# Optimization experiments

Measured on AMD Instinct MI355X. Metric: run time of the kernel, lower is better.

## Reference

```python
import jax, jax.numpy as jnp
import numpy as np

B, T, IN, H, L, OUT, PRED, FN = 512, 96, 64, 512, 2, 1, 24, 32


def setup_inputs() -> dict:
    key = jax.random.key(0)
    ks = jax.random.split(key, 12)
    sc = 0.02
    n = lambda i, shape: jax.random.normal(ks[i], shape, jnp.float32) * sc
    return {
        "x": jax.random.normal(ks[0], (B, T, IN), jnp.float32),
        "station_id": jax.random.randint(ks[1], (B,), 0, 26, jnp.int32),
        "W_hidden": n(2, (H, IN)), "b_hidden": jnp.zeros((H,), jnp.float32),
        "embed": n(3, (26, H)),
        "W_ih": n(4, (L, 4 * H, H)), "W_hh": n(5, (L, 4 * H, H)),
        "b_ih": jnp.zeros((L, 4 * H), jnp.float32), "b_hh": jnp.zeros((L, 4 * H), jnp.float32),
        "conv_W": n(6, (FN, T - 1)), "conv_b": jnp.zeros((FN,), jnp.float32),
        "W1": n(7, (FN, H)), "b1": jnp.zeros((FN,), jnp.float32),
        "W2": n(8, (H, H + FN)), "b2": jnp.zeros((H,), jnp.float32),
        "W_out": n(9, (T * OUT, H)), "b_out": jnp.zeros((T * OUT,), jnp.float32),
    }


def _lstm(xc, W_ih, W_hh, b_ih, b_hh):
    # xc: [B, T, H]; multi-layer LSTM, PyTorch gate order i,f,g,o
    n_layers = W_ih.shape[0]
    h0 = jnp.zeros((n_layers, xc.shape[0], W_hh.shape[-1]), xc.dtype)

    def step(carry, xt):
        h, c = carry  # [L, B, H]
        inp = xt
        hs, cs = [], []
        for l in range(n_layers):
            g = inp @ W_ih[l].T + h[l] @ W_hh[l].T + b_ih[l] + b_hh[l]
            i, f, gg, o = jnp.split(g, 4, axis=-1)
            cn = jax.nn.sigmoid(f) * c[l] + jax.nn.sigmoid(i) * jnp.tanh(gg)
            hn = jax.nn.sigmoid(o) * jnp.tanh(cn)
            hs.append(hn); cs.append(cn)
            inp = hn
        return (jnp.stack(hs), jnp.stack(cs)), inp  # emit last-layer h

    _, outs = jax.lax.scan(step, (h0, h0), jnp.swapaxes(xc, 0, 1))
    return jnp.swapaxes(outs, 0, 1)  # [B, T, H] last-layer hidden states


def reference(x, station_id, W_hidden, b_hidden, embed, W_ih, W_hh, b_ih, b_hh,
              conv_W, conv_b, W1, b1, W2, b2, W_out, b_out):
    b, t, _ = x.shape
    hdim = W_hidden.shape[0]
    fn = conv_W.shape[0]
    xc = jax.nn.relu(x @ W_hidden.T + b_hidden)
    xc = xc + embed[station_id][:, None, :]
    hs_seq = _lstm(xc, W_ih, W_hh, b_ih, b_hh)          # [B, T, H]
    Hmat = jax.nn.relu(hs_seq[:, :-1, :])                # [B, T-1, H]
    htt = hs_seq[:, -1, :]                               # [B, H]
    # Conv2d(1, FN, (T-1, 1)) over [B,1,T-1,H] == contraction over time
    conv = jax.nn.relu(jnp.einsum('bth,ft->bfh', Hmat, conv_W) + conv_b[None, :, None])
    # original does .view(-1, feat_size, filter_num): raw reshape, not transpose
    feat = conv.reshape(b, hdim, fn)                     # [B, H, FN]
    w = (htt @ W1.T + b1)[:, None, :]                    # [B, 1, FN]
    alpha = jax.nn.sigmoid(jnp.sum(feat * w, axis=2))    # [B, H]
    v = jnp.sum(alpha[:, :, None] * feat, axis=1)        # [B, FN]
    new_ht = jnp.concatenate([htt, v], axis=1) @ W2.T + b2
    ypred = (new_ht @ W_out.T + b_out)[:, -PRED * OUT:]
    return ypred
```

## Files before the change

kernel.cpp:

```cpp
#include <hip/hip_runtime.h>
#include <math.h>

namespace {

constexpr int B = 512, T = 96, IN = 64, H = 512, G4 = 2048;
constexpr int FN = 32, KC = 544, NPRED = 24, TM1 = T - 1;
constexpr int BH = B * H;

typedef __attribute__((ext_vector_type(8))) short s8v;
typedef __attribute__((ext_vector_type(16))) float f16v;

__device__ __forceinline__ float sigf(float x) { return 1.0f / (1.0f + __expf(-x)); }
__device__ __forceinline__ float tanhfast(float x) {
  x = fminf(fmaxf(x, -15.f), 15.f);
  float e = __expf(2.0f * x);
  return (e - 1.0f) / (e + 1.0f);
}
__device__ __forceinline__ unsigned short bf16_rne(float f) {
  unsigned u = __float_as_uint(f);
  u += 0x7fffu + ((u >> 16) & 1u);
  return (unsigned short)(u >> 16);
}
__device__ __forceinline__ void split8(const float4& x, const float4& y, s8v& hi, s8v& lo) {
  float vs[8] = {x.x, x.y, x.z, x.w, y.x, y.y, y.z, y.w};
#pragma unroll
  for (int j = 0; j < 8; ++j) {
    unsigned ub = __float_as_uint(vs[j]);
    hi[j] = (short)(ub >> 16);
    lo[j] = (short)bf16_rne(vs[j] - __uint_as_float(ub & 0xffff0000u));
  }
}

__global__ __launch_bounds__(256) void k_xc(
    const float* __restrict__ x, const int* __restrict__ sid,
    const float* __restrict__ Wh, const float* __restrict__ bh,
    const float* __restrict__ emb, float* __restrict__ planes) {
  constexpr int RWS = 64;
  int gid = blockIdx.x;
  int half = gid & 1;
  int row0 = (gid >> 1) * RWS;
  int tid = threadIdx.x;
  int h = half * 256 + tid;
  __shared__ float sx[RWS][IN];
  {
    const float4* xsrc = (const float4*)(x + (size_t)row0 * IN);
    float4* sdst = (float4*)(&sx[0][0]);
    for (int i = tid; i < RWS * IN / 4; i += 256) sdst[i] = xsrc[i];
  }
  float4 w[16];
  const float* wr = Wh + (size_t)h * IN;
#pragma unroll
  for (int j = 0; j < 16; ++j) w[j] = *(const float4*)(wr + j * 4);
  float b0 = bh[h];
  const float* ep = emb + h;
  __syncthreads();
#pragma unroll 2
  for (int r = 0; r < RWS; ++r) {
    float a0 = b0, a1 = 0.f, a2 = 0.f, a3 = 0.f;
#pragma unroll
    for (int j = 0; j < 16; ++j) {
      float4 xv = *(const float4*)(&sx[r][j * 4]);
      a0 = fmaf(xv.x, w[j].x, a0);
      a1 = fmaf(xv.y, w[j].y, a1);
      a2 = fmaf(xv.z, w[j].z, a2);
      a3 = fmaf(xv.w, w[j].w, a3);
    }
    float acc = (a0 + a1) + (a2 + a3);
    int row = row0 + r;
    int bb = row / T, t = row % T;
    float v = fmaxf(acc, 0.f) + ep[(size_t)sid[bb] * H];
    planes[((size_t)t * B + bb) * H + h] = v;
  }
}

__global__ __launch_bounds__(256) void k_wswz(
    const float* __restrict__ Wih, const float* __restrict__ Whh,
    short* __restrict__ WFhi, short* __restrict__ WFlo) {
  int g = blockIdx.x * 256 + threadIdx.x;
  int lane = g & 63;
  int fi = g >> 6;
  int nt = fi & 3, kt = (fi >> 2) & 63, ng = (fi >> 8) & 15, layer = fi >> 12;
  int row = nt * H + ng * 32 + (lane & 31);
  int kk = kt * 16 + (lane >> 5) * 8;
  const float* src = (kk < H) ? (Wih + ((size_t)layer * G4 + row) * H + kk)
                              : (Whh + ((size_t)layer * G4 + row) * H + (kk - H));
  float4 f0 = *(const float4*)src, f1 = *(const float4*)(src + 4);
  s8v hi, lo;
  split8(f0, f1, hi, lo);
  size_t o = (size_t)fi * 512 + lane * 8;
  *(s8v*)(WFhi + o) = hi;
  *(s8v*)(WFlo + o) = lo;
}

__global__ __launch_bounds__(256, 1) void k_step(
    int tt, float* __restrict__ planes, const short* __restrict__ WFhi,
    const short* __restrict__ WFlo, short* __restrict__ hFhi,
    short* __restrict__ hFlo, const float* __restrict__ bih,
    const float* __restrict__ bhh, float* __restrict__ c0,
    float* __restrict__ c1) {
  int gid = blockIdx.x;
  int xcd = gid & 7;
  int u = gid >> 3;
  int combo = xcd * 4 + (u & 3);
  int layer = combo >> 4;
  if (layer ? (tt == 0) : (tt == T)) return;
  int ng = combo & 15;
  int b0 = (u >> 2) * 64;
  int step = layer ? (tt - 1) : tt;
  int tid = threadIdx.x, lane = tid & 63, wk = tid >> 6;
  int l31 = lane & 31, lh = lane >> 5;

  __shared__ float comb[4][4][32][32];

  const float* bi = bih + (size_t)layer * G4;
  const float* bh2 = bhh + (size_t)layer * G4;
  float* cbuf = layer ? c1 : c0;

  int rpar = (step - 1) & 1;
  const float* xbase = nullptr;
  const short *abhi = nullptr, *ablo = nullptr;
  if (layer == 0 && wk < 2) {
    xbase = planes + (size_t)step * BH + (size_t)(b0 + l31) * H + wk * 256 + lh * 8;
  } else {
    int src = (layer == 0) ? 0 : ((wk < 2) ? 0 : 1);
    int par = (layer == 0) ? rpar : ((wk < 2) ? (step & 1) : rpar);
    int kk0 = wk * 16 - ((layer == 0 || wk >= 2) ? 32 : 0);
    size_t o = ((((size_t)src * 2 + par) * 32 + kk0) * H + (b0 + l31)) * 16 + lh * 8;
    abhi = hFhi + o;
    ablo = hFlo + o;
  }

  float bias[4];
#pragma unroll
  for (int nt = 0; nt < 4; ++nt) {
    int r = nt * H + ng * 32 + l31;
    bias[nt] = bi[r] + bh2[r];
  }

  const size_t wstep = 4 * 512;
  const size_t wbase0 = ((size_t)(layer * 16 + ng) * 64 + wk * 16) * wstep + (size_t)lane * 8;
  const size_t astep = (size_t)H * 16;

  f16v acc[2][4];
#pragma unroll
  for (int rt = 0; rt < 2; ++rt)
#pragma unroll
    for (int nt = 0; nt < 4; ++nt)
#pragma unroll
      for (int e = 0; e < 16; ++e) acc[rt][nt][e] = 0.f;

  s8v a0h0, a0l0, a0h1, a0l1, b0h0, b0h1, b0h2, b0h3, b0l0, b0l1, b0l2, b0l3;
  s8v a1h0, a1l0, a1h1, a1l1, b1h0, b1h1, b1h2, b1h3, b1l0, b1l1, b1l2, b1l3;
  s8v a2h0, a2l0, a2h1, a2l1, b2h0, b2h1, b2h2, b2h3, b2l0, b2l1, b2l2, b2l3;

#define LOADW_(kq, bh0, bh1, bh2, bh3, bl0, bl1, bl2, bl3)          \
  {                                                                 \
    size_t wo = wbase0 + (size_t)(kq) * wstep;                      \
    bh0 = *(const s8v*)(WFhi + wo);                                 \
    bh1 = *(const s8v*)(WFhi + wo + 512);                           \
    bh2 = *(const s8v*)(WFhi + wo + 1024);                          \
    bh3 = *(const s8v*)(WFhi + wo + 1536);                          \
    bl0 = *(const s8v*)(WFlo + wo);                                 \
    bl1 = *(const s8v*)(WFlo + wo + 512);                           \
    bl2 = *(const s8v*)(WFlo + wo + 1024);                          \
    bl3 = *(const s8v*)(WFlo + wo + 1536);                          \
  }
#define LOADA_(kq, ah0, al0, ah1, al1)                              \
  {                                                                 \
    if (xbase) {                                                    \
      const float* ap = xbase + (kq) * 16;                          \
      float4 f0 = *(const float4*)ap, f1 = *(const float4*)(ap + 4);\
      split8(f0, f1, ah0, al0);                                     \
      const float* aq = ap + 32 * H;                                \
      float4 g0 = *(const float4*)aq, g1 = *(const float4*)(aq + 4);\
      split8(g0, g1, ah1, al1);                                     \
    } else {                                                        \
      const short* ph = abhi + (size_t)(kq) * astep;                \
      const short* pl = ablo + (size_t)(kq) * astep;                \
      ah0 = *(const s8v*)(ph);                                      \
      al0 = *(const s8v*)(pl);                                      \
      ah1 = *(const s8v*)(ph + 512);                                \
      al1 = *(const s8v*)(pl + 512);                                \
    }                                                               \
  }
#define MFMA3R_(rt, ah, al, bh0, bh1, bh2, bh3, bl0, bl1, bl2, bl3)                        \
  {                                                                                        \
    acc[rt][0] = __builtin_amdgcn_mfma_f32_32x32x16_bf16(ah, bh0, acc[rt][0], 0, 0, 0);    \
    acc[rt][1] = __builtin_amdgcn_mfma_f32_32x32x16_bf16(ah, bh1, acc[rt][1], 0, 0, 0);    \
    acc[rt][2] = __builtin_amdgcn_mfma_f32_32x32x16_bf16(ah, bh2, acc[rt][2], 0, 0, 0);    \
    acc[rt][3] = __builtin_amdgcn_mfma_f32_32x32x16_bf16(ah, bh3, acc[rt][3], 0, 0, 0);    \
    acc[rt][0] = __builtin_amdgcn_mfma_f32_32x32x16_bf16(ah, bl0, acc[rt][0], 0, 0, 0);    \
    acc[rt][1] = __builtin_amdgcn_mfma_f32_32x32x16_bf16(ah, bl1, acc[rt][1], 0, 0, 0);    \
    acc[rt][2] = __builtin_amdgcn_mfma_f32_32x32x16_bf16(ah, bl2, acc[rt][2], 0, 0, 0);    \
    acc[rt][3] = __builtin_amdgcn_mfma_f32_32x32x16_bf16(ah, bl3, acc[rt][3], 0, 0, 0);    \
    acc[rt][0] = __builtin_amdgcn_mfma_f32_32x32x16_bf16(al, bh0, acc[rt][0], 0, 0, 0);    \
    acc[rt][1] = __builtin_amdgcn_mfma_f32_32x32x16_bf16(al, bh1, acc[rt][1], 0, 0, 0);    \
    acc[rt][2] = __builtin_amdgcn_mfma_f32_32x32x16_bf16(al, bh2, acc[rt][2], 0, 0, 0);    \
    acc[rt][3] = __builtin_amdgcn_mfma_f32_32x32x16_bf16(al, bh3, acc[rt][3], 0, 0, 0);    \
  }
#define MFMA6_(ah0, al0, ah1, al1, bh0, bh1, bh2, bh3, bl0, bl1, bl2, bl3)  \
  {                                                                         \
    MFMA3R_(0, ah0, al0, bh0, bh1, bh2, bh3, bl0, bl1, bl2, bl3);           \
    MFMA3R_(1, ah1, al1, bh0, bh1, bh2, bh3, bl0, bl1, bl2, bl3);           \
  }

  LOADA_(0, a0h0, a0l0, a0h1, a0l1);
  LOADW_(0, b0h0, b0h1, b0h2, b0h3, b0l0, b0l1, b0l2, b0l3);
  LOADA_(1, a1h0, a1l0, a1h1, a1l1);
  LOADW_(1, b1h0, b1h1, b1h2, b1h3, b1l0, b1l1, b1l2, b1l3);
  LOADA_(2, a2h0, a2l0, a2h1, a2l1);
  LOADW_(2, b2h0, b2h1, b2h2, b2h3, b2l0, b2l1, b2l2, b2l3);
#pragma unroll 1
  for (int kp = 0; kp < 5; ++kp) {
    int kq = kp * 3;
    MFMA6_(a0h0, a0l0, a0h1, a0l1, b0h0, b0h1, b0h2, b0h3, b0l0, b0l1, b0l2, b0l3);
    LOADA_(kq + 3, a0h0, a0l0, a0h1, a0l1);
    LOADW_(kq + 3, b0h0, b0h1, b0h2, b0h3, b0l0, b0l1, b0l2, b0l3);
    MFMA6_(a1h0, a1l0, a1h1, a1l1, b1h0, b1h1, b1h2, b1h3, b1l0, b1l1, b1l2, b1l3);
    if (kp < 4) {
      LOADA_(kq + 4, a1h0, a1l0, a1h1, a1l1);
      LOADW_(kq + 4, b1h0, b1h1, b1h2, b1h3, b1l0, b1l1, b1l2, b1l3);
    }
    MFMA6_(a2h0, a2l0, a2h1, a2l1, b2h0, b2h1, b2h2, b2h3, b2l0, b2l1, b2l2, b2l3);
    if (kp < 4) {
      LOADA_(kq + 5, a2h0, a2l0, a2h1, a2l1);
      LOADW_(kq + 5, b2h0, b2h1, b2h2, b2h3, b2l0, b2l1, b2l2, b2l3);
    }
  }
  MFMA6_(a0h0, a0l0, a0h1, a0l1, b0h0, b0h1, b0h2, b0h3, b0l0, b0l1, b0l2, b0l3);
#undef LOADW_
#undef LOADA_
#undef MFMA3R_
#undef MFMA6_

#pragma unroll
  for (int rt = 0; rt < 2; ++rt) {
    if (rt) __syncthreads();
#pragma unroll
    for (int nt = 0; nt < 4; ++nt)
#pragma unroll
      for (int r = 0; r < 16; ++r) {
        int row = (r & 3) + 8 * (r >> 2) + 4 * lh;
        comb[nt][wk][row][l31] = acc[rt][nt][r];
      }
    __syncthreads();
    int b0p = b0 + rt * 32;
#pragma unroll
    for (int rr = 0; rr < 4; ++rr) {
      int r = wk * 4 + rr;
      int row = (r & 3) + 8 * (r >> 2) + 4 * lh;
      float g[4];
#pragma unroll
      for (int nt = 0; nt < 4; ++nt) {
        float p0 = comb[nt][0][row][l31];
        float p1 = comb[nt][1][row][l31];
        float p2 = comb[nt][2][row][l31];
        float p3 = comb[nt][3][row][l31];
        g[nt] = (p0 + p1) + (p2 + p3) + bias[nt];
      }
      size_t coff = (size_t)(b0p + row) * H + ng * 32 + l31;
      float cp = cbuf[coff];
      float cn = sigf(g[1]) * cp + sigf(g[0]) * tanhfast(g[2]);
      float hn = sigf(g[3]) * tanhfast(cn);
      cbuf[coff] = cn;
      int brow = b0p + row;
      int hcol = ng * 32 + l31;
      size_t o = ((((size_t)layer * 2 + (step & 1)) * 32 + (hcol >> 4)) * H + brow) * 16 + (hcol & 15);
      unsigned ub = __float_as_uint(hn);
      hFhi[o] = (short)(ub >> 16);
      hFlo[o] = (short)bf16_rne(hn - __uint_as_float(ub & 0xffff0000u));
      if (layer) planes[(size_t)step * BH + (size_t)brow * H + hcol] = hn;
    }
  }
}

__global__ __launch_bounds__(256) void k_conv(
    const float* __restrict__ hs, const float* __restrict__ cW,
    const float* __restrict__ cb, float* __restrict__ feat) {
  int b = blockIdx.x >> 2;
  int h0 = (blockIdx.x & 3) * 128;
  int tid = threadIdx.x;
  __shared__ float sW[TM1][FN];
  for (int i = tid; i < TM1 * FN; i += 256) sW[i >> 5][i & 31] = cW[(i & 31) * TM1 + (i >> 5)];
  __syncthreads();
  int hl = tid & 127, fg = (tid >> 7) * 16;
  float acc[16];
#pragma unroll
  for (int j = 0; j < 16; ++j) acc[j] = cb[fg + j];
  const float* hp = hs + (size_t)b * H + h0 + hl;
  for (int t = 0; t < TM1; ++t) {
    float v = fmaxf(hp[(size_t)t * BH], 0.f);
#pragma unroll
    for (int j = 0; j < 16; ++j) acc[j] = fmaf(v, sW[t][fg + j], acc[j]);
  }
#pragma unroll
  for (int j = 0; j < 16; ++j)
    feat[(size_t)b * (FN * H) + (size_t)(fg + j) * H + h0 + hl] = fmaxf(acc[j], 0.f);
}

__global__ __launch_bounds__(256) void k_attn(
    const float* __restrict__ hs, const float* __restrict__ feat,
    const float* __restrict__ W1, const float* __restrict__ b1,
    const float* __restrict__ W2, const float* __restrict__ b2,
    const float* __restrict__ Wout, const float* __restrict__ bout,
    float* __restrict__ out) {
  int b = blockIdx.x, tid = threadIdx.x;
  __shared__ float sh[H], sa[H], snew[H], sw[FN], sv[FN], red[256];
  const float* htt = hs + (size_t)(T - 1) * BH + (size_t)b * H;
  for (int i = tid; i < H; i += 256) sh[i] = htt[i];
  __syncthreads();
  {
    int f = tid >> 3, sl = tid & 7;
    const float* w1 = W1 + (size_t)f * H;
    float p = 0.f;
    for (int k = sl * 64; k < sl * 64 + 64; ++k) p = fmaf(sh[k], w1[k], p);
    p += __shfl_xor(p, 1); p += __shfl_xor(p, 2); p += __shfl_xor(p, 4);
    if (sl == 0) sw[f] = p + b1[f];
  }
  __syncthreads();
  const float* fb = feat + (size_t)b * (FN * H);
  for (int i = tid; i < H; i += 256) {
    const float* fr = fb + (size_t)i * FN;
    float p = 0.f;
#pragma unroll
    for (int j = 0; j < FN; j += 4) {
      float4 fv = *(const float4*)(fr + j);
      p = fmaf(fv.x, sw[j], p);
      p = fmaf(fv.y, sw[j + 1], p);
      p = fmaf(fv.z, sw[j + 2], p);
      p = fmaf(fv.w, sw[j + 3], p);
    }
    sa[i] = sigf(p);
  }
  __syncthreads();
  {
    int j = tid & 31, isl = tid >> 5;
    float p = 0.f;
    for (int i = isl * 64; i < isl * 64 + 64; ++i) p = fmaf(sa[i], fb[(size_t)i * FN + j], p);
    red[tid] = p;
  }
  __syncthreads();
  if (tid < 128) red[tid] += red[tid + 128];
  __syncthreads();
  if (tid < 64) red[tid] += red[tid + 64];
  __syncthreads();
  if (tid < 32) sv[tid] = red[tid] + red[tid + 32];
  __syncthreads();
  for (int h = tid; h < H; h += 256) {
    const float* w2 = W2 + (size_t)h * KC;
    float p = b2[h];
#pragma unroll 4
    for (int k = 0; k < H; k += 4) {
      float4 wv = *(const float4*)(w2 + k);
      float4 shv = *(const float4*)(sh + k);
      p = fmaf(shv.x, wv.x, p);
      p = fmaf(shv.y, wv.y, p);
      p = fmaf(shv.z, wv.z, p);
      p = fmaf(shv.w, wv.w, p);
    }
#pragma unroll
    for (int j = 0; j < FN; j += 4) {
      float4 wv = *(const float4*)(w2 + H + j);
      p = fmaf(sv[j], wv.x, p);
      p = fmaf(sv[j + 1], wv.y, p);
      p = fmaf(sv[j + 2], wv.z, p);
      p = fmaf(sv[j + 3], wv.w, p);
    }
    snew[h] = p;
  }
  __syncthreads();
  if (tid < NPRED * 8) {
    int p = tid >> 3, sl = tid & 7;
    const float* wo = Wout + (size_t)(T - NPRED + p) * H;
    float sacc = 0.f;
    for (int k = sl * 64; k < sl * 64 + 64; ++k) sacc = fmaf(snew[k], wo[k], sacc);
    sacc += __shfl_xor(sacc, 1); sacc += __shfl_xor(sacc, 2); sacc += __shfl_xor(sacc, 4);
    if (sl == 0) out[(size_t)b * NPRED + p] = sacc + bout[T - NPRED + p];
  }
}

}

extern "C" void kernel_launch(void* const* d_in, const int* in_sizes, int n_in,
                              void* d_out, int out_size, void* d_ws, size_t ws_size,
                              hipStream_t stream) {
  const float* x    = (const float*)d_in[0];
  const int*   sid  = (const int*)d_in[1];
  const float* Wh   = (const float*)d_in[2];
  const float* bh   = (const float*)d_in[3];
  const float* emb  = (const float*)d_in[4];
  const float* Wih  = (const float*)d_in[5];
  const float* Whh  = (const float*)d_in[6];
  const float* bih  = (const float*)d_in[7];
  const float* bhh  = (const float*)d_in[8];
  const float* cW   = (const float*)d_in[9];
  const float* cb   = (const float*)d_in[10];
  const float* W1   = (const float*)d_in[11];
  const float* b1   = (const float*)d_in[12];
  const float* W2   = (const float*)d_in[13];
  const float* b2   = (const float*)d_in[14];
  const float* Wout = (const float*)d_in[15];
  const float* bout = (const float*)d_in[16];
  float* out = (float*)d_out;

  constexpr size_t HFE = (size_t)2 * 2 * 32 * H * 16;
  float* planes = (float*)d_ws;
  short* WFhi = (short*)(planes + (size_t)T * BH);
  short* WFlo = WFhi + (size_t)8192 * 512;
  short* hFhi = WFlo + (size_t)8192 * 512;
  short* hFlo = hFhi + HFE;
  float* cst = (float*)(hFlo + HFE);
  float* c0 = cst;
  float* c1 = cst + BH;
  float* feat = c1 + BH;
  size_t need = (size_t)T * BH * 4 + (size_t)8192 * 512 * 2 * 2 + HFE * 2 * 2 +
                2 * (size_t)BH * 4 + (size_t)B * FN * H * 4;
  if (ws_size < need) return;

  hipMemsetAsync(hFhi, 0, HFE * 2 * 2 + 2 * (size_t)BH * 4, stream);
  k_xc<<<(B * T / 64) * 2, 256, 0, stream>>>(x, sid, Wh, bh, emb, planes);
  k_wswz<<<2048, 256, 0, stream>>>(Wih, Whh, WFhi, WFlo);

  for (int tt = 0; tt <= T; ++tt)
    k_step<<<256, 256, 0, stream>>>(tt, planes, WFhi, WFlo, hFhi, hFlo, bih, bhh, c0, c1);

  k_conv<<<B * 4, 256, 0, stream>>>(planes, cW, cb, feat);
  k_attn<<<B, 256, 0, stream>>>(planes, feat, W1, b1, W2, b2, Wout, bout, out);
}
```

Before: 2.324 ms.

## Transpose W2 for coalesced reads, fuse attention passes, widen xc per-thread work

Adds a kernel that transposes W2 into a k-group-major float4 layout, so the W2 matvec in the attention kernel reads coalesced across threads instead of strided by row. The alpha computation and the weighted feature sum are fused into a single pass that uses shuffle reductions plus a float4 tree reduction, which removes the sa buffer and a second read of feat. k_xc now computes both halves of H per thread, so each x row is loaded into shared memory once instead of twice, at the cost of higher register use. These kernels are small next to the 97 sequential LSTM step launches.

```diff
diff --git a/kernel.cpp b/kernel.cpp
--- a/kernel.cpp
+++ b/kernel.cpp
@@ -36,40 +36,48 @@
     const float* __restrict__ Wh, const float* __restrict__ bh,
     const float* __restrict__ emb, float* __restrict__ planes) {
   constexpr int RWS = 64;
-  int gid = blockIdx.x;
-  int half = gid & 1;
-  int row0 = (gid >> 1) * RWS;
+  int row0 = blockIdx.x * RWS;
   int tid = threadIdx.x;
-  int h = half * 256 + tid;
-  __shared__ float sx[RWS][IN];
+  __shared__ __align__(16) float sx[RWS][IN];
   {
     const float4* xsrc = (const float4*)(x + (size_t)row0 * IN);
     float4* sdst = (float4*)(&sx[0][0]);
     for (int i = tid; i < RWS * IN / 4; i += 256) sdst[i] = xsrc[i];
   }
-  float4 w[16];
-  const float* wr = Wh + (size_t)h * IN;
-#pragma unroll
-  for (int j = 0; j < 16; ++j) w[j] = *(const float4*)(wr + j * 4);
-  float b0 = bh[h];
-  const float* ep = emb + h;
+  float4 w0[16], w1[16];
+  const float* wr0 = Wh + (size_t)tid * IN;
+  const float* wr1 = Wh + (size_t)(tid + 256) * IN;
+#pragma unroll
+  for (int j = 0; j < 16; ++j) {
+    w0[j] = *(const float4*)(wr0 + j * 4);
+    w1[j] = *(const float4*)(wr1 + j * 4);
+  }
+  float bb0 = bh[tid], bb1 = bh[tid + 256];
   __syncthreads();
 #pragma unroll 2
   for (int r = 0; r < RWS; ++r) {
-    float a0 = b0, a1 = 0.f, a2 = 0.f, a3 = 0.f;
+    float a00 = bb0, a01 = 0.f, a02 = 0.f, a03 = 0.f;
+    float a10 = bb1, a11 = 0.f, a12 = 0.f, a13 = 0.f;
 #pragma unroll
     for (int j = 0; j < 16; ++j) {
       float4 xv = *(const float4*)(&sx[r][j * 4]);
-      a0 = fmaf(xv.x, w[j].x, a0);
-      a1 = fmaf(xv.y, w[j].y, a1);
-      a2 = fmaf(xv.z, w[j].z, a2);
-      a3 = fmaf(xv.w, w[j].w, a3);
-    }
-    float acc = (a0 + a1) + (a2 + a3);
+      a00 = fmaf(xv.x, w0[j].x, a00);
+      a01 = fmaf(xv.y, w0[j].y, a01);
+      a02 = fmaf(xv.z, w0[j].z, a02);
+      a03 = fmaf(xv.w, w0[j].w, a03);
+      a10 = fmaf(xv.x, w1[j].x, a10);
+      a11 = fmaf(xv.y, w1[j].y, a11);
+      a12 = fmaf(xv.z, w1[j].z, a12);
+      a13 = fmaf(xv.w, w1[j].w, a13);
+    }
+    float acc0 = (a00 + a01) + (a02 + a03);
+    float acc1 = (a10 + a11) + (a12 + a13);
     int row = row0 + r;
     int bb = row / T, t = row % T;
-    float v = fmaxf(acc, 0.f) + ep[(size_t)sid[bb] * H];
-    planes[((size_t)t * B + bb) * H + h] = v;
+    const float* eb = emb + (size_t)sid[bb] * H;
+    size_t o = ((size_t)t * B + bb) * H;
+    planes[o + tid] = fmaxf(acc0, 0.f) + eb[tid];
+    planes[o + tid + 256] = fmaxf(acc1, 0.f) + eb[tid + 256];
   }
 }
 
@@ -92,6 +100,13 @@
   *(s8v*)(WFlo + o) = lo;
 }
 
+__global__ __launch_bounds__(256) void k_w2t(
+    const float* __restrict__ W2, float* __restrict__ W2T4) {
+  int g = blockIdx.x * 256 + threadIdx.x;
+  int h = g / KC, k = g % KC;
+  W2T4[((size_t)(k >> 2) * H + h) * 4 + (k & 3)] = W2[g];
+}
+
 __global__ __launch_bounds__(256, 1) void k_step(
     int tt, float* __restrict__ planes, const short* __restrict__ WFhi,
     const short* __restrict__ WFlo, short* __restrict__ hFhi,
@@ -175,12 +190,12 @@
       float4 g0 = *(const float4*)aq, g1 = *(const float4*)(aq + 4);\
       split8(g0, g1, ah1, al1);                                     \
     } else {                                                        \
-      const short* ph = abhi + (size_t)(kq) * astep;                \
-      const short* pl = ablo + (size_t)(kq) * astep;                \
-      ah0 = *(const s8v*)(ph);                                      \
-      al0 = *(const s8v*)(pl);                                      \
-      ah1 = *(const s8v*)(ph + 512);                                \
-      al1 = *(const s8v*)(pl + 512);                                \
+      const short* ph_ = abhi + (size_t)(kq) * astep;               \
+      const short* pl_ = ablo + (size_t)(kq) * astep;               \
+      ah0 = *(const s8v*)(ph_);                                     \
+      al0 = *(const s8v*)(pl_);                                     \
+      ah1 = *(const s8v*)(ph_ + 512);                               \
+      al1 = *(const s8v*)(pl_ + 512);                               \
     }                                                               \
   }
 #define MFMA3R_(rt, ah, al, bh0, bh1, bh2, bh3, bl0, bl1, bl2, bl3)                        \
@@ -301,11 +316,12 @@
 __global__ __launch_bounds__(256) void k_attn(
     const float* __restrict__ hs, const float* __restrict__ feat,
     const float* __restrict__ W1, const float* __restrict__ b1,
-    const float* __restrict__ W2, const float* __restrict__ b2,
+    const float* __restrict__ W2T4, const float* __restrict__ b2,
     const float* __restrict__ Wout, const float* __restrict__ bout,
     float* __restrict__ out) {
   int b = blockIdx.x, tid = threadIdx.x;
-  __shared__ float sh[H], sa[H], snew[H], sw[FN], sv[FN], red[256];
+  __shared__ __align__(16) float sh[H], snew[H], sw[FN], sv[FN];
+  __shared__ __align__(16) float4 red4[32][8];
   const float* htt = hs + (size_t)(T - 1) * BH + (size_t)b * H;
   for (int i = tid; i < H; i += 256) sh[i] = htt[i];
   __syncthreads();
@@ -319,52 +335,60 @@
   }
   __syncthreads();
   const float* fb = feat + (size_t)b * (FN * H);
-  for (int i = tid; i < H; i += 256) {
-    const float* fr = fb + (size_t)i * FN;
-    float p = 0.f;
-#pragma unroll
-    for (int j = 0; j < FN; j += 4) {
-      float4 fv = *(const float4*)(fr + j);
-      p = fmaf(fv.x, sw[j], p);
-      p = fmaf(fv.y, sw[j + 1], p);
-      p = fmaf(fv.z, sw[j + 2], p);
-      p = fmaf(fv.w, sw[j + 3], p);
-    }
-    sa[i] = sigf(p);
-  }
-  __syncthreads();
-  {
-    int j = tid & 31, isl = tid >> 5;
-    float p = 0.f;
-    for (int i = isl * 64; i < isl * 64 + 64; ++i) p = fmaf(sa[i], fb[(size_t)i * FN + j], p);
-    red[tid] = p;
-  }
-  __syncthreads();
-  if (tid < 128) red[tid] += red[tid + 128];
-  __syncthreads();
-  if (tid < 64) red[tid] += red[tid + 64];
-  __syncthreads();
-  if (tid < 32) sv[tid] = red[tid] + red[tid + 32];
-  __syncthreads();
-  for (int h = tid; h < H; h += 256) {
-    const float* w2 = W2 + (size_t)h * KC;
+  int ig = tid >> 3, j0 = (tid & 7) * 4;
+  float4 swv = *(const float4*)(&sw[j0]);
+  float4 vacc = {0.f, 0.f, 0.f, 0.f};
+#pragma unroll 4
+  for (int p = 0; p < 16; ++p) {
+    int i = p * 32 + ig;
+    float4 f4 = *(const float4*)(fb + (size_t)i * FN + j0);
+    float s = f4.x * swv.x;
+    s = fmaf(f4.y, swv.y, s);
+    s = fmaf(f4.z, swv.z, s);
+    s = fmaf(f4.w, swv.w, s);
+    s += __shfl_xor(s, 1); s += __shfl_xor(s, 2); s += __shfl_xor(s, 4);
+    s = sigf(s);
+    vacc.x = fmaf(s, f4.x, vacc.x);
+    vacc.y = fmaf(s, f4.y, vacc.y);
+    vacc.z = fmaf(s, f4.z, vacc.z);
+    vacc.w = fmaf(s, f4.w, vacc.w);
+  }
+  red4[ig][tid & 7] = vacc;
+  __syncthreads();
+#pragma unroll
+  for (int s2 = 16; s2 >= 1; s2 >>= 1) {
+    if (tid < s2 * 8) {
+      float4 a = red4[tid >> 3][tid & 7];
+      float4 c = red4[(tid >> 3) + s2][tid & 7];
+      a.x += c.x; a.y += c.y; a.z += c.z; a.w += c.w;
+      red4[tid >> 3][tid & 7] = a;
+    }
+    __syncthreads();
+  }
+  if (tid < FN) sv[tid] = ((const float*)&red4[0][0])[tid];
+  __syncthreads();
+#pragma unroll
+  for (int q = 0; q < 2; ++q) {
+    int h = tid + q * 256;
     float p = b2[h];
+    const float* wt = W2T4 + (size_t)h * 4;
 #pragma unroll 4
-    for (int k = 0; k < H; k += 4) {
-      float4 wv = *(const float4*)(w2 + k);
-      float4 shv = *(const float4*)(sh + k);
+    for (int kg = 0; kg < 128; ++kg) {
+      float4 wv = *(const float4*)(wt + (size_t)kg * (H * 4));
+      float4 shv = *(const float4*)(&sh[kg * 4]);
       p = fmaf(shv.x, wv.x, p);
       p = fmaf(shv.y, wv.y, p);
       p = fmaf(shv.z, wv.z, p);
       p = fmaf(shv.w, wv.w, p);
     }
 #pragma unroll
-    for (int j = 0; j < FN; j += 4) {
-      float4 wv = *(const float4*)(w2 + H + j);
-      p = fmaf(sv[j], wv.x, p);
-      p = fmaf(sv[j + 1], wv.y, p);
-      p = fmaf(sv[j + 2], wv.z, p);
-      p = fmaf(sv[j + 3], wv.w, p);
+    for (int kg = 128; kg < 136; ++kg) {
+      float4 wv = *(const float4*)(wt + (size_t)kg * (H * 4));
+      float4 svv = *(const float4*)(&sv[(kg - 128) * 4]);
+      p = fmaf(svv.x, wv.x, p);
+      p = fmaf(svv.y, wv.y, p);
+      p = fmaf(svv.z, wv.z, p);
+      p = fmaf(svv.w, wv.w, p);
     }
     snew[h] = p;
   }
@@ -413,17 +437,19 @@
   float* c0 = cst;
   float* c1 = cst + BH;
   float* feat = c1 + BH;
+  float* w2t4 = feat + (size_t)B * FN * H;
   size_t need = (size_t)T * BH * 4 + (size_t)8192 * 512 * 2 * 2 + HFE * 2 * 2 +
-                2 * (size_t)BH * 4 + (size_t)B * FN * H * 4;
+                2 * (size_t)BH * 4 + (size_t)B * FN * H * 4 + (size_t)KC * H * 4;
   if (ws_size < need) return;
 
   hipMemsetAsync(hFhi, 0, HFE * 2 * 2 + 2 * (size_t)BH * 4, stream);
-  k_xc<<<(B * T / 64) * 2, 256, 0, stream>>>(x, sid, Wh, bh, emb, planes);
+  k_xc<<<B * T / 64, 256, 0, stream>>>(x, sid, Wh, bh, emb, planes);
   k_wswz<<<2048, 256, 0, stream>>>(Wih, Whh, WFhi, WFlo);
+  k_w2t<<<(H * KC) / 256, 256, 0, stream>>>(W2, w2t4);
 
   for (int tt = 0; tt <= T; ++tt)
     k_step<<<256, 256, 0, stream>>>(tt, planes, WFhi, WFlo, hFhi, hFlo, bih, bhh, c0, c1);
 
   k_conv<<<B * 4, 256, 0, stream>>>(planes, cW, cb, feat);
-  k_attn<<<B, 256, 0, stream>>>(planes, feat, W1, b1, W2, b2, Wout, bout, out);
-}
+  k_attn<<<B, 256, 0, stream>>>(planes, feat, W1, b1, w2t4, b2, Wout, bout, out);
+}
```

Result: faster. 2.255 ms, median of 2 (-3.0%).
